# Kernel optimization log

Measured on AMD Instinct MI355X. Metric: run time of the kernel, lower is better.

The kernel has to match this reference:

```python
import jax, jax.numpy as jnp
import numpy as np

B, N, H = 2, 2048, 256
NUM_HEADS = 8
HEAD_DIM = H // NUM_HEADS
E = 65536
NEG = -1e30
LN_EPS = 1e-5


def setup_inputs() -> dict:
    key = jax.random.key(0)
    ks = jax.random.split(key, 8)
    x = jax.random.normal(ks[0], (B, N, H), dtype=jnp.float32)
    edge_index = jax.random.randint(ks[1], (2, E), 0, N, dtype=jnp.int32)
    edge_weights = jax.random.uniform(ks[2], (E,), dtype=jnp.float32)
    s = 1.0 / np.sqrt(H)
    Wq = jax.random.normal(ks[3], (H, H), dtype=jnp.float32) * s
    Wk = jax.random.normal(ks[4], (H, H), dtype=jnp.float32) * s
    Wv = jax.random.normal(ks[5], (H, H), dtype=jnp.float32) * s
    Wo = jax.random.normal(ks[6], (H, H), dtype=jnp.float32) * s
    ln_gamma = jnp.ones((H,), dtype=jnp.float32)
    ln_beta = jnp.zeros((H,), dtype=jnp.float32)
    return {"node_embeddings": x, "edge_index": edge_index, "edge_weights": edge_weights,
            "Wq": Wq, "Wk": Wk, "Wv": Wv, "Wo": Wo, "ln_gamma": ln_gamma, "ln_beta": ln_beta}


def reference(node_embeddings, edge_index, edge_weights, Wq, Wk, Wv, Wo, ln_gamma, ln_beta):
    x = node_embeddings
    residual = x
    # torch Linear: y = x @ W.T
    def proj(W):
        y = jnp.einsum('bnd,ed->bne', x, W)
        return y.reshape(B, N, NUM_HEADS, HEAD_DIM).transpose(0, 2, 1, 3)  # [B,h,N,hd]
    Q, K, V = proj(Wq), proj(Wk), proj(Wv)
    scale = 1.0 / jnp.sqrt(jnp.float32(HEAD_DIM))
    scores = jnp.einsum('bhnd,bhmd->bhnm', Q, K) * scale  # [B,h,N,N]
    # adjacency mask from edge list
    mask = jnp.zeros((N, N), dtype=bool).at[edge_index[0], edge_index[1]].set(True)
    scores = jnp.where(mask[None, None], scores, NEG)
    w = jax.nn.softmax(scores, axis=-1)
    # rows with no edges: softmax over uniform NEG -> uniform; multiply by mask zeroes them
    # (equivalent to torch's -inf softmax + nan->0, but grad-safe)
    w = w * mask[None, None].astype(w.dtype)
    attn = jnp.einsum('bhnm,bhmd->bhnd', w, V)
    attn = attn.transpose(0, 2, 1, 3).reshape(B, N, H)
    out = jnp.einsum('bnd,ed->bne', attn, Wo)
    y = out + residual
    mu = jnp.mean(y, axis=-1, keepdims=True)
    var = jnp.mean(jnp.square(y - mu), axis=-1, keepdims=True)
    y = (y - mu) / jnp.sqrt(var + LN_EPS) * ln_gamma + ln_beta
    return y
```

## Files before the change

kernel.cpp:

```cpp
#include <hip/hip_runtime.h>
#include <math.h>

#define Bb 2
#define Nn 2048
#define Hh 256
#define NH 8
#define HD 32
#define NEDGE 65536
#define LN_EPS 1e-5f
#define MW 64

typedef __bf16 bf16_t;
typedef bf16_t bf16x8 __attribute__((ext_vector_type(8)));
typedef bf16_t bf16x4 __attribute__((ext_vector_type(4)));
typedef float f32x4 __attribute__((ext_vector_type(4)));

__global__ void build_mask_kernel(const int* __restrict__ ei, unsigned int* __restrict__ mask) {
    int e = blockIdx.x * blockDim.x + threadIdx.x;
    if (e >= NEDGE) return;
    int src = ei[e];
    int dst = ei[NEDGE + e];
    atomicOr(&mask[src * MW + (dst >> 5)], 1u << (dst & 31));
}

__global__ __launch_bounds__(256) void cvt_bf16_kernel(
    const float* __restrict__ s0, const float* __restrict__ s1, const float* __restrict__ s2,
    const float* __restrict__ s3, const float* __restrict__ s4,
    bf16_t* __restrict__ d0, bf16_t* __restrict__ d1, bf16_t* __restrict__ d2,
    bf16_t* __restrict__ d3, bf16_t* __restrict__ d4)
{
    int which = blockIdx.y;
    const float* s = (which == 0) ? s0 : (which == 1) ? s1 : (which == 2) ? s2 : (which == 3) ? s3 : s4;
    bf16_t* d = (which == 0) ? d0 : (which == 1) ? d1 : (which == 2) ? d2 : (which == 3) ? d3 : d4;
    int n4 = (which == 0) ? (Bb * Nn * Hh / 4) : (Hh * Hh / 4);
    int i = blockIdx.x * blockDim.x + threadIdx.x;
    if (i >= n4) return;
    float4 v = ((const float4*)s)[i];
    bf16x4 o = {(bf16_t)v.x, (bf16_t)v.y, (bf16_t)v.z, (bf16_t)v.w};
    ((bf16x4*)d)[i] = o;
}

#define LDA2 72

__global__ __launch_bounds__(256) void qkv_gemm2_kernel(
    const bf16_t* __restrict__ xb,
    const bf16_t* __restrict__ Wqb, const bf16_t* __restrict__ Wkb, const bf16_t* __restrict__ Wvb,
    float* __restrict__ Qb, float* __restrict__ Kb, float* __restrict__ Vb)
{
    __shared__ bf16_t As[64 * LDA2];
    __shared__ bf16_t Ws[64 * LDA2];
    int t = threadIdx.x;
    int lane = t & 63, w = t >> 6;
    int wm = w & 1, wn = w >> 1;
    int ml = lane & 15, quad = lane >> 4;
    int m0 = blockIdx.x * 64;
    int wsel = blockIdx.y >> 2;
    const bf16_t* W = (wsel == 0) ? Wqb : ((wsel == 1) ? Wkb : Wvb);
    float* Ob = (wsel == 0) ? Qb : ((wsel == 1) ? Kb : Vb);
    int n0 = (blockIdx.y & 3) * 64;
    int srow = t >> 3;
    int scol = (t & 7) * 8;
    f32x4 acc[2][2];
    f32x4 zero = {0.f, 0.f, 0.f, 0.f};
    acc[0][0] = zero; acc[0][1] = zero; acc[1][0] = zero; acc[1][1] = zero;

    for (int k0 = 0; k0 < Hh; k0 += 64) {
        bf16x8 a[2], b[2];
        #pragma unroll
        for (int s = 0; s < 2; ++s) {
            a[s] = *(const bf16x8*)(xb + (size_t)(m0 + srow + s * 32) * Hh + k0 + scol);
            b[s] = *(const bf16x8*)(W  + (size_t)(n0 + srow + s * 32) * Hh + k0 + scol);
        }
        __syncthreads();
        #pragma unroll
        for (int s = 0; s < 2; ++s) {
            *(bf16x8*)&As[(srow + s * 32) * LDA2 + scol] = a[s];
            *(bf16x8*)&Ws[(srow + s * 32) * LDA2 + scol] = b[s];
        }
        __syncthreads();
        #pragma unroll
        for (int kk = 0; kk < 64; kk += 32) {
            bf16x8 af[2], bfr[2];
            #pragma unroll
            for (int i = 0; i < 2; ++i) {
                af[i]  = *(const bf16x8*)&As[(wm * 32 + i * 16 + ml) * LDA2 + kk + quad * 8];
                bfr[i] = *(const bf16x8*)&Ws[(wn * 32 + i * 16 + ml) * LDA2 + kk + quad * 8];
            }
            #pragma unroll
            for (int i = 0; i < 2; ++i)
                #pragma unroll
                for (int j = 0; j < 2; ++j)
                    acc[i][j] = __builtin_amdgcn_mfma_f32_16x16x32_bf16(af[i], bfr[j], acc[i][j], 0, 0, 0);
        }
    }
    #pragma unroll
    for (int i = 0; i < 2; ++i)
        #pragma unroll
        for (int j = 0; j < 2; ++j)
            #pragma unroll
            for (int r = 0; r < 4; ++r) {
                int mg = m0 + wm * 32 + i * 16 + quad * 4 + r;
                int ng = n0 + wn * 32 + j * 16 + ml;
                Ob[(size_t)mg * Hh + ng] = acc[i][j][r];
            }
}

__global__ __launch_bounds__(256) void attn4_kernel(
    const float* __restrict__ Qb, const float* __restrict__ Kb, const float* __restrict__ Vb,
    const unsigned int* __restrict__ mask, float* __restrict__ attn)
{
    __shared__ unsigned short nbr[Nn];
    __shared__ float qs[Hh];
    __shared__ float sraw[32 * 9];
    __shared__ float scw[Hh];
    __shared__ int nn_sh;
    int gid = blockIdx.x;
    int i = gid & (Nn - 1);
    int b = gid >> 11;
    int t = threadIdx.x;
    int h = t >> 5, dl = t & 31;
    int w = t >> 6, lane = t & 63;

    if (t < 64) {
        unsigned int bits = mask[i * MW + t];
        int cnt = __popc(bits);
        int incl = cnt;
        #pragma unroll
        for (int off = 1; off < 64; off <<= 1) {
            int v = __shfl_up(incl, off, 64);
            if (t >= off) incl += v;
        }
        int idx = incl - cnt;
        unsigned int bb = bits;
        while (bb) {
            int bit = __ffs(bb) - 1;
            nbr[idx++] = (unsigned short)(t * 32 + bit);
            bb &= bb - 1;
        }
        if (t == 63) nn_sh = incl;
    }
    qs[t] = Qb[((size_t)((b << 11) + i)) * Hh + t];
    __syncthreads();
    int nn = nn_sh;

    float m_run = -1e30f, l_run = 0.f, o = 0.f;
    const float scale = 0.17677669529663687f;
    int nch = (nn + 31) >> 5;
    for (int c = 0; c < nch; ++c) {
        int base = c << 5;
        int lim = min(32, nn - base);
        float4 qv = *(const float4*)&qs[lane << 2];
        #pragma unroll
        for (int s = 0; s < 8; ++s) {
            int r = (s << 2) + w;
            if (r < lim) {
                int j = nbr[base + r];
                float4 kv = *(const float4*)(Kb + (((size_t)((b << 11) + j)) << 8) + (lane << 2));
                float p = fmaf(kv.x, qv.x, fmaf(kv.y, qv.y, fmaf(kv.z, qv.z, kv.w * qv.w)));
                p += __shfl_xor(p, 1, 64);
                p += __shfl_xor(p, 2, 64);
                p += __shfl_xor(p, 4, 64);
                if ((lane & 7) == 0) sraw[r * 9 + (lane >> 3)] = p * scale;
            }
        }
        __syncthreads();
        float s_val = (dl < lim) ? sraw[dl * 9 + h] : -1e30f;
        float mc = s_val;
        #pragma unroll
        for (int m = 1; m < 32; m <<= 1) mc = fmaxf(mc, __shfl_xor(mc, m, 64));
        float m_new = fmaxf(m_run, mc);
        float wgt = __expf(s_val - m_new);
        float sum = wgt;
        #pragma unroll
        for (int m = 1; m < 32; m <<= 1) sum += __shfl_xor(sum, m, 64);
        float alpha = __expf(m_run - m_new);
        l_run = l_run * alpha + sum;
        m_run = m_new;
        scw[t] = wgt;
        __syncthreads();
        float oc0 = 0.f, oc1 = 0.f, oc2 = 0.f, oc3 = 0.f;
        int kl = 0;
        for (; kl + 4 <= lim; kl += 4) {
            int j0 = nbr[base + kl + 0], j1 = nbr[base + kl + 1];
            int j2 = nbr[base + kl + 2], j3 = nbr[base + kl + 3];
            float w0 = scw[(h << 5) + kl + 0], w1 = scw[(h << 5) + kl + 1];
            float w2 = scw[(h << 5) + kl + 2], w3 = scw[(h << 5) + kl + 3];
            float v0 = Vb[(((size_t)((b << 11) + j0)) << 8) + t];
            float v1 = Vb[(((size_t)((b << 11) + j1)) << 8) + t];
            float v2 = Vb[(((size_t)((b << 11) + j2)) << 8) + t];
            float v3 = Vb[(((size_t)((b << 11) + j3)) << 8) + t];
            oc0 = fmaf(w0, v0, oc0); oc1 = fmaf(w1, v1, oc1);
            oc2 = fmaf(w2, v2, oc2); oc3 = fmaf(w3, v3, oc3);
        }
        for (; kl < lim; ++kl) {
            int j = nbr[base + kl];
            oc0 = fmaf(scw[(h << 5) + kl], Vb[(((size_t)((b << 11) + j)) << 8) + t], oc0);
        }
        o = o * alpha + ((oc0 + oc1) + (oc2 + oc3));
    }
    float inv = (l_run > 0.f) ? 1.f / l_run : 0.f;
    attn[((size_t)((b << 11) + i)) * Hh + t] = o * inv;
}

__global__ __launch_bounds__(256) void out_ln_kernel(
    const float* __restrict__ attnb, const bf16_t* __restrict__ Wob,
    const float* __restrict__ x, const float* __restrict__ gamma,
    const float* __restrict__ beta, float* __restrict__ out)
{
    __shared__ bf16_t As[16 * LDA2];
    __shared__ __align__(16) char wbuf[256 * LDA2 * sizeof(bf16_t)];
    bf16_t* Ws = (bf16_t*)wbuf;
    float* yb = (float*)wbuf;
    int t = threadIdx.x;
    int lane = t & 63, w = t >> 6;
    int ml = lane & 15, quad = lane >> 4;
    int m0 = blockIdx.x * 16;
    f32x4 acc[4];
    f32x4 zero = {0.f, 0.f, 0.f, 0.f};
    acc[0] = zero; acc[1] = zero; acc[2] = zero; acc[3] = zero;
    int arow = t >> 4, acol = (t & 15) * 4;
    int wrow = t >> 3, wcol = (t & 7) * 8;

    for (int k0 = 0; k0 < Hh; k0 += 64) {
        float4 av = *(const float4*)(attnb + (size_t)(m0 + arow) * Hh + k0 + acol);
        bf16x8 wv[8];
        #pragma unroll
        for (int s = 0; s < 8; ++s)
            wv[s] = *(const bf16x8*)(Wob + (size_t)(wrow + s * 32) * Hh + k0 + wcol);
        __syncthreads();
        bf16x4 ac = {(bf16_t)av.x, (bf16_t)av.y, (bf16_t)av.z, (bf16_t)av.w};
        *(bf16x4*)&As[arow * LDA2 + acol] = ac;
        #pragma unroll
        for (int s = 0; s < 8; ++s)
            *(bf16x8*)&Ws[(wrow + s * 32) * LDA2 + wcol] = wv[s];
        __syncthreads();
        #pragma unroll
        for (int kk = 0; kk < 64; kk += 32) {
            bf16x8 af = *(const bf16x8*)&As[ml * LDA2 + kk + quad * 8];
            #pragma unroll
            for (int ct = 0; ct < 4; ++ct) {
                bf16x8 bfr = *(const bf16x8*)&Ws[(w * 64 + ct * 16 + ml) * LDA2 + kk + quad * 8];
                acc[ct] = __builtin_amdgcn_mfma_f32_16x16x32_bf16(af, bfr, acc[ct], 0, 0, 0);
            }
        }
    }
    __syncthreads();
    #pragma unroll
    for (int ct = 0; ct < 4; ++ct)
        #pragma unroll
        for (int r = 0; r < 4; ++r) {
            int row = quad * 4 + r;
            int col = w * 64 + ct * 16 + ml;
            yb[row * 260 + col] = acc[ct][r] + x[(size_t)(m0 + row) * Hh + col];
        }
    __syncthreads();
    for (int rr = 0; rr < 4; ++rr) {
        int row = w * 4 + rr;
        float4 v = *(const float4*)&yb[row * 260 + lane * 4];
        float sum = v.x + v.y + v.z + v.w;
        #pragma unroll
        for (int m = 1; m < 64; m <<= 1) sum += __shfl_xor(sum, m, 64);
        float mu = sum * (1.f / Hh);
        float4 d = {v.x - mu, v.y - mu, v.z - mu, v.w - mu};
        float ss = d.x * d.x + d.y * d.y + d.z * d.z + d.w * d.w;
        #pragma unroll
        for (int m = 1; m < 64; m <<= 1) ss += __shfl_xor(ss, m, 64);
        float r = rsqrtf(ss * (1.f / Hh) + LN_EPS);
        float4 g  = *(const float4*)(gamma + lane * 4);
        float4 bt = *(const float4*)(beta + lane * 4);
        float4 ov = {d.x * r * g.x + bt.x, d.y * r * g.y + bt.y,
                     d.z * r * g.z + bt.z, d.w * r * g.w + bt.w};
        *(float4*)(out + (size_t)(m0 + row) * Hh + lane * 4) = ov;
    }
}

extern "C" void kernel_launch(void* const* d_in, const int* in_sizes, int n_in,
                              void* d_out, int out_size, void* d_ws, size_t ws_size,
                              hipStream_t stream) {
    const float* x     = (const float*)d_in[0];
    const int*   ei    = (const int*)d_in[1];
    const float* Wq    = (const float*)d_in[3];
    const float* Wk    = (const float*)d_in[4];
    const float* Wv    = (const float*)d_in[5];
    const float* Wo    = (const float*)d_in[6];
    const float* gamma = (const float*)d_in[7];
    const float* beta  = (const float*)d_in[8];
    float* out = (float*)d_out;

    const int NTOK = Bb * Nn * Hh;
    float* Qb    = (float*)d_ws;
    float* Kb    = Qb + NTOK;
    float* Vb    = Kb + NTOK;
    float* attnb = Vb + NTOK;
    unsigned int* mask = (unsigned int*)(attnb + NTOK);
    bf16_t* xb  = (bf16_t*)(mask + Nn * MW);
    bf16_t* Wqb = xb + NTOK;
    bf16_t* Wkb = Wqb + Hh * Hh;
    bf16_t* Wvb = Wkb + Hh * Hh;
    bf16_t* Wob = Wvb + Hh * Hh;

    hipMemsetAsync(mask, 0, Nn * MW * sizeof(unsigned int), stream);
    hipLaunchKernelGGL(cvt_bf16_kernel, dim3(NTOK / 4 / 256, 5), dim3(256), 0, stream,
                       x, Wq, Wk, Wv, Wo, xb, Wqb, Wkb, Wvb, Wob);
    hipLaunchKernelGGL(build_mask_kernel, dim3(NEDGE / 256), dim3(256), 0, stream, ei, mask);
    hipLaunchKernelGGL(qkv_gemm2_kernel, dim3((Bb * Nn) / 64, 12), dim3(256), 0, stream,
                       xb, Wqb, Wkb, Wvb, Qb, Kb, Vb);
    hipLaunchKernelGGL(attn4_kernel, dim3(Bb * Nn), dim3(256), 0, stream,
                       Qb, Kb, Vb, mask, attnb);
    hipLaunchKernelGGL(out_ln_kernel, dim3((Bb * Nn) / 16), dim3(256), 0, stream,
                       attnb, Wob, x, gamma, beta, out);
}
```

Before: 120.0 us.

## Store K/V in bf16, vectorize V gather per neighbor, fold mask memset into convert kernel

The QKV GEMM now writes K and V as bf16 instead of fp32, which halves the gather traffic in the attention kernel. The attention V accumulation is restructured so each wave handles whole neighbor rows with 4-wide bf16 loads, matching the K path. Per-wave partial outputs are then combined through shared memory, and the online-softmax rescale factors are shared per head. The mask memset is folded into the conversion kernel as an extra grid slice to save one launch. The cost is bf16 rounding of K and V, plus an extra shared-memory reduction step.

```diff
diff --git a/kernel.cpp b/kernel.cpp
--- a/kernel.cpp
+++ b/kernel.cpp
@@ -23,17 +23,22 @@
     atomicOr(&mask[src * MW + (dst >> 5)], 1u << (dst & 31));
 }
 
-__global__ __launch_bounds__(256) void cvt_bf16_kernel(
+__global__ __launch_bounds__(256) void cvt_zero_kernel(
     const float* __restrict__ s0, const float* __restrict__ s1, const float* __restrict__ s2,
     const float* __restrict__ s3, const float* __restrict__ s4,
     bf16_t* __restrict__ d0, bf16_t* __restrict__ d1, bf16_t* __restrict__ d2,
-    bf16_t* __restrict__ d3, bf16_t* __restrict__ d4)
+    bf16_t* __restrict__ d3, bf16_t* __restrict__ d4,
+    uint4* __restrict__ mask4)
 {
     int which = blockIdx.y;
+    int i = blockIdx.x * blockDim.x + threadIdx.x;
+    if (which == 5) {
+        if (i < Nn * MW / 4) mask4[i] = make_uint4(0, 0, 0, 0);
+        return;
+    }
     const float* s = (which == 0) ? s0 : (which == 1) ? s1 : (which == 2) ? s2 : (which == 3) ? s3 : s4;
     bf16_t* d = (which == 0) ? d0 : (which == 1) ? d1 : (which == 2) ? d2 : (which == 3) ? d3 : d4;
     int n4 = (which == 0) ? (Bb * Nn * Hh / 4) : (Hh * Hh / 4);
-    int i = blockIdx.x * blockDim.x + threadIdx.x;
     if (i >= n4) return;
     float4 v = ((const float4*)s)[i];
     bf16x4 o = {(bf16_t)v.x, (bf16_t)v.y, (bf16_t)v.z, (bf16_t)v.w};
@@ -42,10 +47,10 @@
 
 #define LDA2 72
 
-__global__ __launch_bounds__(256) void qkv_gemm2_kernel(
+__global__ __launch_bounds__(256) void qkv_gemm3_kernel(
     const bf16_t* __restrict__ xb,
     const bf16_t* __restrict__ Wqb, const bf16_t* __restrict__ Wkb, const bf16_t* __restrict__ Wvb,
-    float* __restrict__ Qb, float* __restrict__ Kb, float* __restrict__ Vb)
+    float* __restrict__ Qb, bf16_t* __restrict__ Kb16, bf16_t* __restrict__ Vb16)
 {
     __shared__ bf16_t As[64 * LDA2];
     __shared__ bf16_t Ws[64 * LDA2];
@@ -56,7 +61,6 @@
     int m0 = blockIdx.x * 64;
     int wsel = blockIdx.y >> 2;
     const bf16_t* W = (wsel == 0) ? Wqb : ((wsel == 1) ? Wkb : Wvb);
-    float* Ob = (wsel == 0) ? Qb : ((wsel == 1) ? Kb : Vb);
     int n0 = (blockIdx.y & 3) * 64;
     int srow = t >> 3;
     int scol = (t & 7) * 8;
@@ -93,6 +97,7 @@
                     acc[i][j] = __builtin_amdgcn_mfma_f32_16x16x32_bf16(af[i], bfr[j], acc[i][j], 0, 0, 0);
         }
     }
+    bf16_t* Ob16 = (wsel == 1) ? Kb16 : Vb16;
     #pragma unroll
     for (int i = 0; i < 2; ++i)
         #pragma unroll
@@ -101,18 +106,23 @@
             for (int r = 0; r < 4; ++r) {
                 int mg = m0 + wm * 32 + i * 16 + quad * 4 + r;
                 int ng = n0 + wn * 32 + j * 16 + ml;
-                Ob[(size_t)mg * Hh + ng] = acc[i][j][r];
-            }
-}
-
-__global__ __launch_bounds__(256) void attn4_kernel(
-    const float* __restrict__ Qb, const float* __restrict__ Kb, const float* __restrict__ Vb,
-    const unsigned int* __restrict__ mask, float* __restrict__ attn)
+                float v = acc[i][j][r];
+                if (wsel == 0) Qb[(size_t)mg * Hh + ng] = v;
+                else           Ob16[(size_t)mg * Hh + ng] = (bf16_t)v;
+            }
+}
+
+__global__ __launch_bounds__(256) void attn5_kernel(
+    const float* __restrict__ Qb, const bf16_t* __restrict__ Kb16, const bf16_t* __restrict__ Vb16,
+    const unsigned int* __restrict__ mask, float* __restrict__ attnb)
 {
     __shared__ unsigned short nbr[Nn];
     __shared__ float qs[Hh];
     __shared__ float sraw[32 * 9];
     __shared__ float scw[Hh];
+    __shared__ float alpha_l[NH];
+    __shared__ float linv_l[NH];
+    __shared__ float obuf[4][Hh];
     __shared__ int nn_sh;
     int gid = blockIdx.x;
     int i = gid & (Nn - 1);
@@ -120,6 +130,7 @@
     int t = threadIdx.x;
     int h = t >> 5, dl = t & 31;
     int w = t >> 6, lane = t & 63;
+    int hw = lane >> 3;
 
     if (t < 64) {
         unsigned int bits = mask[i * MW + t];
@@ -143,7 +154,8 @@
     __syncthreads();
     int nn = nn_sh;
 
-    float m_run = -1e30f, l_run = 0.f, o = 0.f;
+    float m_run = -1e30f, l_run = 0.f;
+    float o0 = 0.f, o1 = 0.f, o2 = 0.f, o3 = 0.f;
     const float scale = 0.17677669529663687f;
     int nch = (nn + 31) >> 5;
     for (int c = 0; c < nch; ++c) {
@@ -155,8 +167,9 @@
             int r = (s << 2) + w;
             if (r < lim) {
                 int j = nbr[base + r];
-                float4 kv = *(const float4*)(Kb + (((size_t)((b << 11) + j)) << 8) + (lane << 2));
-                float p = fmaf(kv.x, qv.x, fmaf(kv.y, qv.y, fmaf(kv.z, qv.z, kv.w * qv.w)));
+                bf16x4 kv = *(const bf16x4*)(Kb16 + (((size_t)((b << 11) + j)) << 8) + (lane << 2));
+                float p = fmaf((float)kv.x, qv.x, fmaf((float)kv.y, qv.y,
+                          fmaf((float)kv.z, qv.z, (float)kv.w * qv.w)));
                 p += __shfl_xor(p, 1, 64);
                 p += __shfl_xor(p, 2, 64);
                 p += __shfl_xor(p, 4, 64);
@@ -177,29 +190,32 @@
         l_run = l_run * alpha + sum;
         m_run = m_new;
         scw[t] = wgt;
-        __syncthreads();
-        float oc0 = 0.f, oc1 = 0.f, oc2 = 0.f, oc3 = 0.f;
-        int kl = 0;
-        for (; kl + 4 <= lim; kl += 4) {
-            int j0 = nbr[base + kl + 0], j1 = nbr[base + kl + 1];
-            int j2 = nbr[base + kl + 2], j3 = nbr[base + kl + 3];
-            float w0 = scw[(h << 5) + kl + 0], w1 = scw[(h << 5) + kl + 1];
-            float w2 = scw[(h << 5) + kl + 2], w3 = scw[(h << 5) + kl + 3];
-            float v0 = Vb[(((size_t)((b << 11) + j0)) << 8) + t];
-            float v1 = Vb[(((size_t)((b << 11) + j1)) << 8) + t];
-            float v2 = Vb[(((size_t)((b << 11) + j2)) << 8) + t];
-            float v3 = Vb[(((size_t)((b << 11) + j3)) << 8) + t];
-            oc0 = fmaf(w0, v0, oc0); oc1 = fmaf(w1, v1, oc1);
-            oc2 = fmaf(w2, v2, oc2); oc3 = fmaf(w3, v3, oc3);
-        }
-        for (; kl < lim; ++kl) {
-            int j = nbr[base + kl];
-            oc0 = fmaf(scw[(h << 5) + kl], Vb[(((size_t)((b << 11) + j)) << 8) + t], oc0);
-        }
-        o = o * alpha + ((oc0 + oc1) + (oc2 + oc3));
-    }
-    float inv = (l_run > 0.f) ? 1.f / l_run : 0.f;
-    attn[((size_t)((b << 11) + i)) * Hh + t] = o * inv;
+        if (dl == 0) alpha_l[h] = alpha;
+        __syncthreads();
+        float av = alpha_l[hw];
+        o0 *= av; o1 *= av; o2 *= av; o3 *= av;
+        #pragma unroll
+        for (int s = 0; s < 8; ++s) {
+            int r = (s << 2) + w;
+            if (r < lim) {
+                int j = nbr[base + r];
+                float wg = scw[(hw << 5) + r];
+                bf16x4 vv = *(const bf16x4*)(Vb16 + (((size_t)((b << 11) + j)) << 8) + (lane << 2));
+                o0 = fmaf(wg, (float)vv.x, o0);
+                o1 = fmaf(wg, (float)vv.y, o1);
+                o2 = fmaf(wg, (float)vv.z, o2);
+                o3 = fmaf(wg, (float)vv.w, o3);
+            }
+        }
+    }
+    if (dl == 0) linv_l[h] = (l_run > 0.f) ? 1.f / l_run : 0.f;
+    obuf[w][(lane << 2) + 0] = o0;
+    obuf[w][(lane << 2) + 1] = o1;
+    obuf[w][(lane << 2) + 2] = o2;
+    obuf[w][(lane << 2) + 3] = o3;
+    __syncthreads();
+    float val = obuf[0][t] + obuf[1][t] + obuf[2][t] + obuf[3][t];
+    attnb[(((size_t)((b << 11) + i)) << 8) + t] = val * linv_l[t >> 5];
 }
 
 __global__ __launch_bounds__(256) void out_ln_kernel(
@@ -288,10 +304,10 @@
     float* out = (float*)d_out;
 
     const int NTOK = Bb * Nn * Hh;
-    float* Qb    = (float*)d_ws;
-    float* Kb    = Qb + NTOK;
-    float* Vb    = Kb + NTOK;
-    float* attnb = Vb + NTOK;
+    float*  Qb    = (float*)d_ws;
+    bf16_t* Kb16  = (bf16_t*)(Qb + NTOK);
+    bf16_t* Vb16  = Kb16 + NTOK;
+    float*  attnb = (float*)(Vb16 + NTOK);
     unsigned int* mask = (unsigned int*)(attnb + NTOK);
     bf16_t* xb  = (bf16_t*)(mask + Nn * MW);
     bf16_t* Wqb = xb + NTOK;
@@ -299,14 +315,13 @@
     bf16_t* Wvb = Wkb + Hh * Hh;
     bf16_t* Wob = Wvb + Hh * Hh;
 
-    hipMemsetAsync(mask, 0, Nn * MW * sizeof(unsigned int), stream);
-    hipLaunchKernelGGL(cvt_bf16_kernel, dim3(NTOK / 4 / 256, 5), dim3(256), 0, stream,
-                       x, Wq, Wk, Wv, Wo, xb, Wqb, Wkb, Wvb, Wob);
+    hipLaunchKernelGGL(cvt_zero_kernel, dim3(NTOK / 4 / 256, 6), dim3(256), 0, stream,
+                       x, Wq, Wk, Wv, Wo, xb, Wqb, Wkb, Wvb, Wob, (uint4*)mask);
     hipLaunchKernelGGL(build_mask_kernel, dim3(NEDGE / 256), dim3(256), 0, stream, ei, mask);
-    hipLaunchKernelGGL(qkv_gemm2_kernel, dim3((Bb * Nn) / 64, 12), dim3(256), 0, stream,
-                       xb, Wqb, Wkb, Wvb, Qb, Kb, Vb);
-    hipLaunchKernelGGL(attn4_kernel, dim3(Bb * Nn), dim3(256), 0, stream,
-                       Qb, Kb, Vb, mask, attnb);
+    hipLaunchKernelGGL(qkv_gemm3_kernel, dim3((Bb * Nn) / 64, 12), dim3(256), 0, stream,
+                       xb, Wqb, Wkb, Wvb, Qb, Kb16, Vb16);
+    hipLaunchKernelGGL(attn5_kernel, dim3(Bb * Nn), dim3(256), 0, stream,
+                       Qb, Kb16, Vb16, mask, attnb);
     hipLaunchKernelGGL(out_ln_kernel, dim3((Bb * Nn) / 16), dim3(256), 0, stream,
                        attnb, Wob, x, gamma, beta, out);
 }
```

Result: faster. 116.5 us (-2.9%).
